# Optimization experiments

Hardware: AMD Instinct MI355X
Metric: run time of the kernel (lower is better)

## Reference

```python
import jax, jax.numpy as jnp
import numpy as np

B, T, C, H, NUM_EDGE_TYPES = 2, 512, 256, 8, 16


def setup_inputs() -> dict:
    key = jax.random.key(0)
    ks = jax.random.split(key, 8)
    init = 0.02
    x = jax.random.normal(ks[0], (B, T, C), dtype=jnp.float32)
    bias_matrix = jax.random.randint(ks[1], (B, T, T), 0, NUM_EDGE_TYPES)
    w_attn = jax.random.normal(ks[2], (C, 3 * C), dtype=jnp.float32) * init
    w_proj = jax.random.normal(ks[3], (C, C), dtype=jnp.float32) * init
    w_edge_k = jax.random.normal(ks[4], (C, C), dtype=jnp.float32) * init
    w_edge_v = jax.random.normal(ks[5], (C, C), dtype=jnp.float32) * init
    edge_emb_table = jax.random.normal(ks[6], (NUM_EDGE_TYPES, C), dtype=jnp.float32)
    attn_bias_table = jax.random.normal(ks[7], (NUM_EDGE_TYPES, H), dtype=jnp.float32)
    return {
        "x": x,
        "bias_matrix": bias_matrix,
        "w_attn": w_attn,
        "w_proj": w_proj,
        "w_edge_k": w_edge_k,
        "w_edge_v": w_edge_v,
        "edge_emb_table": edge_emb_table,
        "attn_bias_table": attn_bias_table,
    }


def reference(x, bias_matrix, w_attn, w_proj, w_edge_k, w_edge_v,
              edge_emb_table, attn_bias_table):
    b, t, c = x.shape
    h = attn_bias_table.shape[1]
    e = c // h
    scale = jnp.sqrt(jnp.asarray(e, x.dtype))

    qkv = x @ w_attn                              # (B,T,3C)
    q, k, v = jnp.split(qkv, 3, axis=-1)
    # (B,H,T,E)
    q = q.reshape(b, t, h, e).transpose(0, 2, 1, 3)
    k = k.reshape(b, t, h, e).transpose(0, 2, 1, 3)
    v = v.reshape(b, t, h, e).transpose(0, 2, 1, 3)

    # edge-type embeddings and per-pair k/v modulation, (B,T,T,H,E)
    ee = edge_emb_table[bias_matrix]              # (B,T,T,C)
    e_k = (ee @ w_edge_k).reshape(b, t, t, h, e)
    e_v = (ee @ w_edge_v).reshape(b, t, t, h, e)

    # scores[b,h,i,j] = sum_e q[b,h,i,e] * k[b,h,j,e] * e_k[b, j, i, h, e]
    # (torch: e_k permuted to (B,H,j,i,E), broadcast-multiplied by k then
    #  contracted with q via 'bhie,bhjie->bhij')
    scores = jnp.einsum('bhie,bhje,bjihe->bhij', q, k, e_k) / scale

    causal = jnp.tril(jnp.ones((t, t), dtype=bool))  # (T,T)
    scores = jnp.where(causal, scores, -jnp.inf)

    # edge-type attention bias: (B,T,T,H) -> (B,H,T,T), zeroed above diagonal
    bias = attn_bias_table[bias_matrix].transpose(0, 3, 1, 2)
    bias = jnp.where(causal, bias, jnp.zeros((), bias.dtype))

    attn = jax.nn.softmax(scores + bias, axis=-1)  # (B,H,T,T)

    # y[b,h,i,e] = sum_j attn[b,h,i,j] * v[b,h,j,e] * e_v[b, j, i, h, e]
    y = jnp.einsum('bhij,bhje,bjihe->bhie', attn, v, e_v)
    y = y.transpose(0, 2, 1, 3).reshape(b, t, c)
    return y @ w_proj
```

## Files before the change

kernel.cpp:

```cpp
#include <hip/hip_runtime.h>
#include <hip/hip_bf16.h>
#include <math.h>

#define Bdim 2
#define Tdim 512
#define Cdim 256
#define Hdim 8
#define Edim 32
#define NTYPES 16
#define TI 8
#define JT 128

__global__ __launch_bounds__(256) void pre_kernel(
    const float* __restrict__ A, const float* __restrict__ Bw,
    const float* __restrict__ emb, const float* __restrict__ wk,
    const float* __restrict__ wv,
    float* __restrict__ qT, float* __restrict__ kT, float* __restrict__ vT,
    float* __restrict__ ekt, float* __restrict__ evt)
{
    __shared__ float smem[16 * 34 + 16 * 64];
    int tid = threadIdx.x;

    if (blockIdx.x >= 384) {
        int t = blockIdx.x - 384;
        float* se = smem;
        se[tid] = emb[t * Cdim + tid];
        __syncthreads();
        float a = 0.f, b = 0.f;
        for (int k = 0; k < Cdim; ++k) {
            float ev = se[k];
            a = fmaf(ev, wk[k * Cdim + tid], a);
            b = fmaf(ev, wv[k * Cdim + tid], b);
        }
        ekt[t * Cdim + tid] = a;
        evt[t * Cdim + tid] = b;
        return;
    }

    const int N = 3 * Cdim;
    const int K = Cdim;
    float (*As)[34] = (float(*)[34])smem;
    float (*Bs)[64] = (float(*)[64])(smem + 16 * 34);
    int m0 = (blockIdx.x / 12) * 32;
    int n0 = (blockIdx.x % 12) * 64;
    int tr = tid >> 4, tc = tid & 15;
    float acc[2][4] = {};
    int bkr = tid >> 4, bcq = (tid & 15) * 4;

    for (int k0 = 0; k0 < K; k0 += 16) {
        if (tid < 128) {
            int r = tid >> 2, kq = (tid & 3) * 4;
            float4 av = *(const float4*)(A + (size_t)(m0 + r) * K + k0 + kq);
            As[kq + 0][r] = av.x;
            As[kq + 1][r] = av.y;
            As[kq + 2][r] = av.z;
            As[kq + 3][r] = av.w;
        }
        float4 bv = *(const float4*)(Bw + (size_t)(k0 + bkr) * N + n0 + bcq);
        *(float4*)&Bs[bkr][bcq] = bv;
        __syncthreads();
#pragma unroll
        for (int kk = 0; kk < 16; ++kk) {
            float2 a2 = *(float2*)&As[kk][tr * 2];
            float4 b4 = *(float4*)&Bs[kk][tc * 4];
            acc[0][0] = fmaf(a2.x, b4.x, acc[0][0]);
            acc[0][1] = fmaf(a2.x, b4.y, acc[0][1]);
            acc[0][2] = fmaf(a2.x, b4.z, acc[0][2]);
            acc[0][3] = fmaf(a2.x, b4.w, acc[0][3]);
            acc[1][0] = fmaf(a2.y, b4.x, acc[1][0]);
            acc[1][1] = fmaf(a2.y, b4.y, acc[1][1]);
            acc[1][2] = fmaf(a2.y, b4.z, acc[1][2]);
            acc[1][3] = fmaf(a2.y, b4.w, acc[1][3]);
        }
        __syncthreads();
    }
    int sec = n0 >> 8;
    float* dst = (sec == 0) ? qT : (sec == 1) ? kT : vT;
    int cc0 = (n0 & 255) + tc * 4;
    int h = cc0 >> 5;
    int e0 = cc0 & 31;
#pragma unroll
    for (int i = 0; i < 2; ++i) {
        int m = m0 + tr * 2 + i;
        int bq = m >> 9, t = m & (Tdim - 1);
        float4 val = make_float4(acc[i][0], acc[i][1], acc[i][2], acc[i][3]);
        *(float4*)&dst[(((size_t)bq * Hdim + h) * Tdim + t) * Edim + e0] = val;
    }
}

__global__ __launch_bounds__(512, 4) void attn_kernel(
    const float* __restrict__ qT, const float* __restrict__ kT,
    const float* __restrict__ vT, const int* __restrict__ bm,
    const float* __restrict__ ekt, const float* __restrict__ evt,
    const float* __restrict__ abt, float* __restrict__ y)
{
    __shared__ float kv[JT][32];
    __shared__ float qm[TI][NTYPES][32];
    __shared__ float ss[TI][512];
    __shared__ unsigned int st1pf[Tdim];
    __shared__ float sevt[NTYPES][36];
    __shared__ float sabt[NTYPES];
    __shared__ float sinv[TI];

    float* spart = (float*)ss;

    const int tau = 63 - (blockIdx.x >> 4);
    const int bh = blockIdx.x & 15;
    const int h = bh & (Hdim - 1);
    const int b = bh >> 3;
    const int tid = threadIdx.x;
    const int wave = tid >> 6;
    const int lane = tid & 63;
    const float inv_scale = 0.17677669529663687f;

    const float* qbase = qT + (size_t)bh * Tdim * Edim;
    const float* kbase = kT + (size_t)bh * Tdim * Edim;
    const float* vbase = vT + (size_t)bh * Tdim * Edim;
    const int* bmb = bm + (size_t)b * Tdim * Tdim;

    const int sr0 = tid >> 3;
    const int seq4 = (tid & 7) << 2;
    const int ssw = seq4 ^ ((sr0 & 7) << 2);

    const int i0 = tau * TI;
    const int imax = i0 + TI - 1;
    const int njt = (imax >> 7) + 1;
    const int jmax = njt << 7;

    if (tid < 128) {
        int t = tid >> 3, eq = tid & 7;
        *(float4*)&sevt[t][eq * 4] = *(const float4*)&evt[t * Cdim + h * Edim + eq * 4];
    }
    if (tid < NTYPES) sabt[tid] = abt[tid * Hdim + h];
    if (tid < jmax) {
        const int* rowp = bmb + (size_t)tid * Tdim + i0;
        int4 lo = *(const int4*)rowp;
        int4 hi = *(const int4*)(rowp + 4);
        st1pf[tid] =
            ((unsigned)(lo.x & 15)) | (((unsigned)(lo.y & 15)) << 4) |
            (((unsigned)(lo.z & 15)) << 8) | (((unsigned)(lo.w & 15)) << 12) |
            (((unsigned)(hi.x & 15)) << 16) | (((unsigned)(hi.y & 15)) << 20) |
            (((unsigned)(hi.z & 15)) << 24) | (((unsigned)(hi.w & 15)) << 28);
    }
    *(float4*)&kv[sr0][ssw] = *(const float4*)&kbase[((size_t)sr0 << 5) + seq4];
    *(float4*)&kv[sr0 + 64][ssw] =
        *(const float4*)&kbase[(((size_t)sr0 + 64) << 5) + seq4];
    for (int idx = tid; idx < TI * NTYPES * 8; idx += 512) {
        int eq = idx & 7;
        int t = (idx >> 3) & (NTYPES - 1);
        int r = idx >> 7;
        float4 qv = *(const float4*)&qbase[(size_t)(i0 + r) * Edim + eq * 4];
        float4 ev = *(const float4*)&ekt[t * Cdim + h * Edim + eq * 4];
        float4 o;
        o.x = qv.x * ev.x; o.y = qv.y * ev.y;
        o.z = qv.z * ev.z; o.w = qv.w * ev.w;
        *(float4*)&qm[r][t][(eq << 2) ^ ((t & 7) << 2)] = o;
    }
    __syncthreads();

    for (int jt = 0; jt < njt; ++jt) {
        int j0 = jt << 7;
        const float* nsrc =
            (jt + 1 < njt) ? (kbase + ((size_t)(j0 + 128) << 5)) : vbase;
        float4 n0 = *(const float4*)(nsrc + ((size_t)sr0 << 5) + seq4);
        float4 n1 = *(const float4*)(nsrc + (((size_t)sr0 + 64) << 5) + seq4);

        int jsub = wave & 1;
        int jl = (jsub << 6) + lane;
        int j = j0 + jl;
        const int xsw = (jl & 7) << 2;
        float4 k4[8];
#pragma unroll
        for (int eq = 0; eq < 8; ++eq)
            k4[eq] = *(float4*)&kv[jl][(eq << 2) ^ xsw];
        unsigned tp = st1pf[j];

#pragma unroll
        for (int u = 0; u < 2; ++u) {
            int ii = (wave >> 1) + (u << 2);
            int i = i0 + ii;
            if (j0 + (jsub << 6) > i) continue;
            int t1 = (tp >> (ii * 4)) & 15;
            const int qsw = (t1 & 7) << 2;
            float s0 = 0.f, s1 = 0.f;
#pragma unroll
            for (int eq = 0; eq < 8; ++eq) {
                float4 qv = *(float4*)&qm[ii][t1][(eq << 2) ^ qsw];
                s0 = fmaf(qv.x, k4[eq].x, s0);
                s1 = fmaf(qv.y, k4[eq].y, s1);
                s0 = fmaf(qv.z, k4[eq].z, s0);
                s1 = fmaf(qv.w, k4[eq].w, s1);
            }
            if (j <= i) ss[ii][j] = (s0 + s1) * inv_scale;
        }
        __syncthreads();
        *(float4*)&kv[sr0][ssw] = n0;
        *(float4*)&kv[sr0 + 64][ssw] = n1;
        if (jt + 1 < njt) __syncthreads();
    }

    {
        int ii = wave;
        int i = i0 + ii;
        const int* brow = bmb + (size_t)i * Tdim;
        float tb[8];
        float m = -1e30f;
#pragma unroll
        for (int c = 0; c < 8; ++c) {
            int j = (c << 6) + lane;
            float val = ss[ii][j] + sabt[brow[j] & 15];
            tb[c] = (j <= i) ? val : -1e30f;
            m = fmaxf(m, tb[c]);
        }
        for (int off = 32; off; off >>= 1) m = fmaxf(m, __shfl_xor(m, off));
        float sum = 0.f;
#pragma unroll
        for (int c = 0; c < 8; ++c) {
            int j = (c << 6) + lane;
            float p = __expf(tb[c] - m);
            p = (j <= i) ? p : 0.f;
            sum += p;
            if (j <= i) ss[ii][j] = p;
        }
        for (int off = 32; off; off >>= 1) sum += __shfl_xor(sum, off);
        if (lane == 0) sinv[ii] = 1.0f / sum;
    }
    __syncthreads();

    float4 acc[TI];
#pragma unroll
    for (int ii = 0; ii < TI; ++ii) acc[ii] = make_float4(0.f, 0.f, 0.f, 0.f);
    int gid = tid >> 3;
    int eqg4 = (tid & 7) << 2;
    for (int jt = 0; jt < njt; ++jt) {
        int j0 = jt << 7;
        const bool pf = (jt + 1) < njt;
        float4 n0, n1;
        if (pf) {
            const float* nsrc = vbase + ((size_t)(j0 + 128) << 5);
            n0 = *(const float4*)(nsrc + ((size_t)sr0 << 5) + seq4);
            n1 = *(const float4*)(nsrc + (((size_t)sr0 + 64) << 5) + seq4);
        }
#pragma unroll
        for (int sub = 0; sub < 2; ++sub) {
            int jl = (sub << 6) + gid;
            int j = j0 + jl;
            float4 v4 = *(float4*)&kv[jl][eqg4 ^ ((jl & 7) << 2)];
            unsigned tp = st1pf[j];
#pragma unroll
            for (int ii = 0; ii < TI; ++ii) {
                int i = i0 + ii;
                if (j0 + (sub << 6) > i) continue;
                float p = (j <= i) ? ss[ii][j] : 0.f;
                int t1 = (tp >> (ii * 4)) & 15;
                float4 ev = *(float4*)&sevt[t1][eqg4];
                acc[ii].x = fmaf(p * ev.x, v4.x, acc[ii].x);
                acc[ii].y = fmaf(p * ev.y, v4.y, acc[ii].y);
                acc[ii].z = fmaf(p * ev.z, v4.z, acc[ii].z);
                acc[ii].w = fmaf(p * ev.w, v4.w, acc[ii].w);
            }
        }
        __syncthreads();
        if (pf) {
            *(float4*)&kv[sr0][ssw] = n0;
            *(float4*)&kv[sr0 + 64][ssw] = n1;
            __syncthreads();
        }
    }
#pragma unroll
    for (int ii = 0; ii < TI; ++ii) {
#pragma unroll
        for (int m = 8; m <= 32; m <<= 1) {
            acc[ii].x += __shfl_xor(acc[ii].x, m);
            acc[ii].y += __shfl_xor(acc[ii].y, m);
            acc[ii].z += __shfl_xor(acc[ii].z, m);
            acc[ii].w += __shfl_xor(acc[ii].w, m);
        }
    }
    if (lane < 8) {
#pragma unroll
        for (int ii = 0; ii < TI; ++ii)
            *(float4*)&spart[((wave * TI + ii) << 5) + lane * 4] = acc[ii];
    }
    __syncthreads();
    if (tid < TI * Edim) {
        int ii = tid >> 5, e = tid & 31;
        float yv = 0.f;
#pragma unroll
        for (int w = 0; w < 8; ++w) yv += spart[((w * TI + ii) << 5) + e];
        yv *= sinv[ii];
        y[((size_t)(b * Tdim + i0 + ii)) * Cdim + h * Edim + e] = yv;
    }
}

__global__ __launch_bounds__(256) void proj_gemm_kernel(
    const float* __restrict__ A, const float* __restrict__ Bw,
    float* __restrict__ out)
{
    const int N = Cdim;
    const int K = Cdim;
    __shared__ float As[16][34];
    __shared__ float Bs[16][64];
    int m0 = blockIdx.y * 32;
    int n0 = blockIdx.x * 64;
    int tid = threadIdx.x;
    int tr = tid >> 4, tc = tid & 15;
    float acc[2][4] = {};
    int bkr = tid >> 4, bcq = (tid & 15) * 4;

    for (int k0 = 0; k0 < K; k0 += 16) {
        if (tid < 128) {
            int r = tid >> 2, kq = (tid & 3) * 4;
            float4 av = *(const float4*)(A + (size_t)(m0 + r) * K + k0 + kq);
            As[kq + 0][r] = av.x;
            As[kq + 1][r] = av.y;
            As[kq + 2][r] = av.z;
            As[kq + 3][r] = av.w;
        }
        float4 bv = *(const float4*)(Bw + (size_t)(k0 + bkr) * N + n0 + bcq);
        *(float4*)&Bs[bkr][bcq] = bv;
        __syncthreads();
#pragma unroll
        for (int kk = 0; kk < 16; ++kk) {
            float2 a2 = *(float2*)&As[kk][tr * 2];
            float4 b4 = *(float4*)&Bs[kk][tc * 4];
            acc[0][0] = fmaf(a2.x, b4.x, acc[0][0]);
            acc[0][1] = fmaf(a2.x, b4.y, acc[0][1]);
            acc[0][2] = fmaf(a2.x, b4.z, acc[0][2]);
            acc[0][3] = fmaf(a2.x, b4.w, acc[0][3]);
            acc[1][0] = fmaf(a2.y, b4.x, acc[1][0]);
            acc[1][1] = fmaf(a2.y, b4.y, acc[1][1]);
            acc[1][2] = fmaf(a2.y, b4.z, acc[1][2]);
            acc[1][3] = fmaf(a2.y, b4.w, acc[1][3]);
        }
        __syncthreads();
    }
#pragma unroll
    for (int i = 0; i < 2; ++i) {
        int m = m0 + tr * 2 + i;
        float4 val = make_float4(acc[i][0], acc[i][1], acc[i][2], acc[i][3]);
        *(float4*)&out[(size_t)m * N + n0 + tc * 4] = val;
    }
}

extern "C" void kernel_launch(void* const* d_in, const int* in_sizes, int n_in,
                              void* d_out, int out_size, void* d_ws, size_t ws_size,
                              hipStream_t stream) {
    (void)in_sizes; (void)n_in; (void)out_size; (void)ws_size;
    const float* x = (const float*)d_in[0];
    const int* bias_matrix = (const int*)d_in[1];
    const float* w_attn = (const float*)d_in[2];
    const float* w_proj = (const float*)d_in[3];
    const float* w_edge_k = (const float*)d_in[4];
    const float* w_edge_v = (const float*)d_in[5];
    const float* edge_emb = (const float*)d_in[6];
    const float* attn_bias = (const float*)d_in[7];
    float* out = (float*)d_out;

    const size_t n_qkv = (size_t)Bdim * Hdim * Tdim * Edim;
    float* ws = (float*)d_ws;
    float* qT = ws;
    float* kT = qT + n_qkv;
    float* vT = kT + n_qkv;
    float* y = vT + n_qkv;
    float* ekt = y + (size_t)Bdim * Tdim * Cdim;
    float* evt = ekt + (size_t)NTYPES * Cdim;

    pre_kernel<<<400, 256, 0, stream>>>(x, w_attn, edge_emb, w_edge_k, w_edge_v,
                                        qT, kT, vT, ekt, evt);
    attn_kernel<<<dim3(64 * 16), 512, 0, stream>>>(qT, kT, vT, bias_matrix,
                                                   ekt, evt, attn_bias, y);
    proj_gemm_kernel<<<dim3(4, 32), 256, 0, stream>>>(y, w_proj, out);
}
```

Measured before the change: 131.9 us.

## Read K and V directly from global memory instead of LDS staging

Drops the shared-memory K/V tile and its register-prefetch double buffering. Each thread now loads its K row or V slice straight from global memory, which removes the per-tile __syncthreads barriers and frees 16KB of LDS. It also adds early exits that skip j sub-tiles fully above the causal diagonal. The cost is global or cache loads that are no longer coalesced through LDS (each lane reads a whole 128B K row), and there is no explicit prefetch to hide latency.

```diff
diff --git a/kernel.cpp b/kernel.cpp
--- a/kernel.cpp
+++ b/kernel.cpp
@@ -94,7 +94,6 @@
     const float* __restrict__ ekt, const float* __restrict__ evt,
     const float* __restrict__ abt, float* __restrict__ y)
 {
-    __shared__ float kv[JT][32];
     __shared__ float qm[TI][NTYPES][32];
     __shared__ float ss[TI][512];
     __shared__ unsigned int st1pf[Tdim];
@@ -117,10 +116,6 @@
     const float* kbase = kT + (size_t)bh * Tdim * Edim;
     const float* vbase = vT + (size_t)bh * Tdim * Edim;
     const int* bmb = bm + (size_t)b * Tdim * Tdim;
-
-    const int sr0 = tid >> 3;
-    const int seq4 = (tid & 7) << 2;
-    const int ssw = seq4 ^ ((sr0 & 7) << 2);
 
     const int i0 = tau * TI;
     const int imax = i0 + TI - 1;
@@ -142,9 +137,6 @@
             (((unsigned)(hi.x & 15)) << 16) | (((unsigned)(hi.y & 15)) << 20) |
             (((unsigned)(hi.z & 15)) << 24) | (((unsigned)(hi.w & 15)) << 28);
     }
-    *(float4*)&kv[sr0][ssw] = *(const float4*)&kbase[((size_t)sr0 << 5) + seq4];
-    *(float4*)&kv[sr0 + 64][ssw] =
-        *(const float4*)&kbase[(((size_t)sr0 + 64) << 5) + seq4];
     for (int idx = tid; idx < TI * NTYPES * 8; idx += 512) {
         int eq = idx & 7;
         int t = (idx >> 3) & (NTYPES - 1);
@@ -158,46 +150,42 @@
     }
     __syncthreads();
 
-    for (int jt = 0; jt < njt; ++jt) {
-        int j0 = jt << 7;
-        const float* nsrc =
-            (jt + 1 < njt) ? (kbase + ((size_t)(j0 + 128) << 5)) : vbase;
-        float4 n0 = *(const float4*)(nsrc + ((size_t)sr0 << 5) + seq4);
-        float4 n1 = *(const float4*)(nsrc + (((size_t)sr0 + 64) << 5) + seq4);
-
-        int jsub = wave & 1;
-        int jl = (jsub << 6) + lane;
-        int j = j0 + jl;
-        const int xsw = (jl & 7) << 2;
-        float4 k4[8];
-#pragma unroll
-        for (int eq = 0; eq < 8; ++eq)
-            k4[eq] = *(float4*)&kv[jl][(eq << 2) ^ xsw];
-        unsigned tp = st1pf[j];
-
-#pragma unroll
-        for (int u = 0; u < 2; ++u) {
-            int ii = (wave >> 1) + (u << 2);
-            int i = i0 + ii;
-            if (j0 + (jsub << 6) > i) continue;
-            int t1 = (tp >> (ii * 4)) & 15;
-            const int qsw = (t1 & 7) << 2;
-            float s0 = 0.f, s1 = 0.f;
-#pragma unroll
-            for (int eq = 0; eq < 8; ++eq) {
-                float4 qv = *(float4*)&qm[ii][t1][(eq << 2) ^ qsw];
-                s0 = fmaf(qv.x, k4[eq].x, s0);
-                s1 = fmaf(qv.y, k4[eq].y, s1);
-                s0 = fmaf(qv.z, k4[eq].z, s0);
-                s1 = fmaf(qv.w, k4[eq].w, s1);
+    {
+        const int jsub = wave & 1;
+        const int ii0 = wave >> 1;
+        const int jl = (jsub << 6) + lane;
+        for (int jt = 0; jt < njt; ++jt) {
+            int j0 = jt << 7;
+            if (j0 + (jsub << 6) > imax) break;
+            int j = j0 + jl;
+            unsigned tp = st1pf[j];
+            const float* krow = kbase + ((size_t)j << 5);
+            float4 k4[8];
+#pragma unroll
+            for (int eq = 0; eq < 8; ++eq)
+                k4[eq] = *(const float4*)(krow + eq * 4);
+
+#pragma unroll
+            for (int u = 0; u < 2; ++u) {
+                int ii = ii0 + (u << 2);
+                int i = i0 + ii;
+                if (j0 + (jsub << 6) > i) continue;
+                int t1 = (tp >> (ii * 4)) & 15;
+                const int qsw = (t1 & 7) << 2;
+                float s0 = 0.f, s1 = 0.f;
+#pragma unroll
+                for (int eq = 0; eq < 8; ++eq) {
+                    float4 qv = *(float4*)&qm[ii][t1][(eq << 2) ^ qsw];
+                    s0 = fmaf(qv.x, k4[eq].x, s0);
+                    s1 = fmaf(qv.y, k4[eq].y, s1);
+                    s0 = fmaf(qv.z, k4[eq].z, s0);
+                    s1 = fmaf(qv.w, k4[eq].w, s1);
+                }
+                if (j <= i) ss[ii][j] = (s0 + s1) * inv_scale;
             }
-            if (j <= i) ss[ii][j] = (s0 + s1) * inv_scale;
-        }
-        __syncthreads();
-        *(float4*)&kv[sr0][ssw] = n0;
-        *(float4*)&kv[sr0 + 64][ssw] = n1;
-        if (jt + 1 < njt) __syncthreads();
-    }
+        }
+    }
+    __syncthreads();
 
     {
         int ii = wave;
@@ -230,43 +218,34 @@
     float4 acc[TI];
 #pragma unroll
     for (int ii = 0; ii < TI; ++ii) acc[ii] = make_float4(0.f, 0.f, 0.f, 0.f);
-    int gid = tid >> 3;
-    int eqg4 = (tid & 7) << 2;
-    for (int jt = 0; jt < njt; ++jt) {
-        int j0 = jt << 7;
-        const bool pf = (jt + 1) < njt;
-        float4 n0, n1;
-        if (pf) {
-            const float* nsrc = vbase + ((size_t)(j0 + 128) << 5);
-            n0 = *(const float4*)(nsrc + ((size_t)sr0 << 5) + seq4);
-            n1 = *(const float4*)(nsrc + (((size_t)sr0 + 64) << 5) + seq4);
-        }
-#pragma unroll
-        for (int sub = 0; sub < 2; ++sub) {
-            int jl = (sub << 6) + gid;
-            int j = j0 + jl;
-            float4 v4 = *(float4*)&kv[jl][eqg4 ^ ((jl & 7) << 2)];
-            unsigned tp = st1pf[j];
-#pragma unroll
-            for (int ii = 0; ii < TI; ++ii) {
-                int i = i0 + ii;
-                if (j0 + (sub << 6) > i) continue;
-                float p = (j <= i) ? ss[ii][j] : 0.f;
-                int t1 = (tp >> (ii * 4)) & 15;
-                float4 ev = *(float4*)&sevt[t1][eqg4];
-                acc[ii].x = fmaf(p * ev.x, v4.x, acc[ii].x);
-                acc[ii].y = fmaf(p * ev.y, v4.y, acc[ii].y);
-                acc[ii].z = fmaf(p * ev.z, v4.z, acc[ii].z);
-                acc[ii].w = fmaf(p * ev.w, v4.w, acc[ii].w);
+    {
+        const int gid = tid >> 3;
+        const int eqg4 = (tid & 7) << 2;
+        for (int jt = 0; jt < njt; ++jt) {
+            int j0 = jt << 7;
+#pragma unroll
+            for (int sub = 0; sub < 2; ++sub) {
+                if (j0 + (sub << 6) > imax) continue;
+                int jl = (sub << 6) + gid;
+                int j = j0 + jl;
+                float4 v4 = *(const float4*)&vbase[((size_t)j << 5) + eqg4];
+                unsigned tp = st1pf[j];
+#pragma unroll
+                for (int ii = 0; ii < TI; ++ii) {
+                    int i = i0 + ii;
+                    if (j0 + (sub << 6) > i) continue;
+                    float p = (j <= i) ? ss[ii][j] : 0.f;
+                    int t1 = (tp >> (ii * 4)) & 15;
+                    float4 ev = *(float4*)&sevt[t1][eqg4];
+                    acc[ii].x = fmaf(p * ev.x, v4.x, acc[ii].x);
+                    acc[ii].y = fmaf(p * ev.y, v4.y, acc[ii].y);
+                    acc[ii].z = fmaf(p * ev.z, v4.z, acc[ii].z);
+                    acc[ii].w = fmaf(p * ev.w, v4.w, acc[ii].w);
+                }
             }
         }
-        __syncthreads();
-        if (pf) {
-            *(float4*)&kv[sr0][ssw] = n0;
-            *(float4*)&kv[sr0 + 64][ssw] = n1;
-            __syncthreads();
-        }
-    }
+    }
+    __syncthreads();
 #pragma unroll
     for (int ii = 0; ii < TI; ++ii) {
 #pragma unroll
```

Result: slower. 139.4 us (+5.7%).
